# Performance work log

Hardware: AMD Instinct MI355X
Metric: run time of the kernel (lower is better)

## Reference

```python
import jax, jax.numpy as jnp
import numpy as np

EPS_MIN = 1e-8
N_ITER = 50  # solver_iter


def solve_qp_simplex(M, n_iter=N_ITER):
    """Frank-Wolfe min over the simplex of alpha^T M alpha. M: (B,K,K) -> alpha: (B,K)."""
    B, K, _ = M.shape
    alpha0 = jnp.full((B, K), 1.0 / K, dtype=M.dtype)

    def step(alpha, it):
        grad = 2.0 * jnp.einsum('bij,bj->bi', M, alpha)           # (B,K)
        idx = jnp.argmin(grad, axis=1)                             # (B,)
        s = jax.nn.one_hot(idx, K, dtype=alpha.dtype)              # vertex of simplex
        gamma = 2.0 / (it + 2.0)
        return (1.0 - gamma) * alpha + gamma * s, None

    alpha, _ = jax.lax.scan(step, alpha0, jnp.arange(n_iter, dtype=M.dtype))
    return alpha


def _raw_loss(scores, targets, C):
    B, K = scores.shape
    # epsilon = offdiag_mean of C per batch, scaled by 1.0, clamped
    offdiag_mean = (C.sum(axis=(1, 2)) - jnp.trace(C, axis1=1, axis2=2)) / (K * K - K)
    eps = jnp.maximum(offdiag_mean, EPS_MIN)                       # (B,)

    f = 0.5 * scores
    exponent = -(f[:, :, None] + f[:, None, :] + C) / eps[:, None, None]  # (B,K,K)
    shift = exponent.max(axis=(1, 2), keepdims=True)
    logM = exponent - shift
    M = jnp.exp(logM)

    # solver is an implicit layer: non-differentiable by construction
    alpha = jax.lax.stop_gradient(solve_qp_simplex(M, N_ITER))     # (B,K)

    pos = alpha > 0
    loga = jnp.where(pos, jnp.log(jnp.where(pos, alpha, 1.0)), -jnp.inf)
    term = loga[:, :, None] + loga[:, None, :] + logM              # (B,K,K)
    logval = jax.scipy.special.logsumexp(term.reshape(B, K * K), axis=1)
    conjugate = -eps * (logval + shift.reshape(B))

    f_y = jnp.take_along_axis(scores, targets[:, None], axis=1)[:, 0]
    return conjugate - f_y


def setup_inputs() -> dict:
    key = jax.random.key(0)
    k1, k2, k3 = jax.random.split(key, 3)
    B, K = 512, 256
    scores = jax.random.normal(k1, (B, K), dtype=jnp.float32)
    targets = jax.random.randint(k2, (B,), 0, K)
    C = jax.random.uniform(k3, (B, K, K), dtype=jnp.float32)
    return {"scores": scores, "targets": targets, "C": C}


def reference(scores, targets, C):
    return _raw_loss(scores, targets, C).mean()
```

## Files before the change

### kernel.cpp

```cpp
#include <hip/hip_runtime.h>
#include <hip/hip_fp16.h>
#include <math.h>

#define KDIM 256
#define NITER 50
#define REG_H 8192
#define STR 266


__global__ __launch_bounds__(256, 7) void k1_stream(
    const float* __restrict__ scores, const float* __restrict__ C,
    __half* __restrict__ CT,
    float* __restrict__ psum_o, float* __restrict__ ptrace_o, float* __restrict__ pmin_o)
{
    const int blk = blockIdx.x;
    const int b = blk >> 2, chunk = blk & 3;
    const int tid = threadIdx.x, lane = tid & 63, wave = tid >> 6;
    const float4* C4 = (const float4*)(C + (size_t)b * KDIM * KDIM);
    __half* CTb = CT + (size_t)((b*4 + chunk) * 2) * REG_H;

    __shared__ float sf[KDIM];
    __shared__ __half T[32 * STR];
    __shared__ float redS[256], redT[256], redM[256];

    sf[tid] = 0.5f * scores[b*KDIM + tid];
    __syncthreads();

    const int j0 = lane * 4;
    const float fj0 = sf[j0], fj1 = sf[j0+1], fj2 = sf[j0+2], fj3 = sf[j0+3];

    float psum = 0.f, ptrace = 0.f, pmin = INFINITY;

    #pragma unroll
    for (int p = 0; p < 2; ++p) {
        #pragma unroll
        for (int it = 0; it < 8; ++it) {
            const int sl  = it*4 + wave;
            const int row = chunk*64 + p*32 + sl;
            float4 c4 = C4[row*(KDIM/4) + lane];
            const float frow = sf[row];
            psum += (c4.x + c4.y) + (c4.z + c4.w);
            pmin = fminf(pmin, fminf(fminf(frow+fj0+c4.x, frow+fj1+c4.y),
                                     fminf(frow+fj2+c4.z, frow+fj3+c4.w)));
            if ((row >> 2) == lane) {
                int r2 = row & 3;
                ptrace += (r2==0)?c4.x:(r2==1)?c4.y:(r2==2)?c4.z:c4.w;
            }
            __half2 h01, h23;
            h01.x = __float2half_rn(c4.x); h01.y = __float2half_rn(c4.y);
            h23.x = __float2half_rn(c4.z); h23.y = __float2half_rn(c4.w);
            *(__half2*)&T[sl*STR + j0    ] = h01;
            *(__half2*)&T[sl*STR + j0 + 2] = h23;
        }
        __syncthreads();
        {
            __half* dst = CTb + (size_t)p * REG_H;
            const int jr  = tid >> 2;
            const int sl0 = (tid & 3) * 8;
            #pragma unroll
            for (int r = 0; r < 4; ++r) {
                const int j = r*64 + jr;
                uint w[4];
                #pragma unroll
                for (int dw = 0; dw < 4; ++dw) {
                    const uint u0 = (uint)__half_as_ushort(T[(sl0 + dw*2    )*STR + j]);
                    const uint u1 = (uint)__half_as_ushort(T[(sl0 + dw*2 + 1)*STR + j]);
                    w[dw] = u0 | (u1 << 16);
                }
                uint4 v; v.x = w[0]; v.y = w[1]; v.z = w[2]; v.w = w[3];
                *(uint4*)(dst + (size_t)j*32 + sl0) = v;
            }
        }
        __syncthreads();
    }

    redS[tid] = psum; redT[tid] = ptrace; redM[tid] = pmin;
    __syncthreads();
    for (int s = 128; s > 0; s >>= 1) {
        if (tid < s) {
            redS[tid] += redS[tid+s];
            redT[tid] += redT[tid+s];
            redM[tid]  = fminf(redM[tid], redM[tid+s]);
        }
        __syncthreads();
    }
    if (tid == 0) { psum_o[blk] = redS[0]; ptrace_o[blk] = redT[0]; pmin_o[blk] = redM[0]; }
}

__global__ __launch_bounds__(256, 6) void k2_rowsums(
    const float* __restrict__ scores, const __half* __restrict__ CT,
    const float* __restrict__ psum_i, const float* __restrict__ ptrace_i, const float* __restrict__ pmin_i,
    float* __restrict__ prs)
{
    const int blk = blockIdx.x;
    const int b = blk >> 2, jc = blk & 3;
    const int tid = threadIdx.x, lane = tid & 63, wave = tid >> 6;
    const __half* CTb = CT + (size_t)b * 8 * REG_H;

    __shared__ float sf[KDIM];
    __shared__ float part[12];
    __shared__ float bc2[2];
    __shared__ float racc[4][KDIM];

    sf[tid] = 0.5f * scores[b*KDIM + tid];
    if (tid < 12) {
        part[tid] = (tid < 4) ? psum_i[b*4+tid]
                  : (tid < 8) ? ptrace_i[b*4+tid-4]
                              : pmin_i[b*4+tid-8];
    }
    __syncthreads();
    if (tid == 0) {
        float s = part[0]+part[1]+part[2]+part[3];
        float t = part[4]+part[5]+part[6]+part[7];
        float mn = fminf(fminf(part[8],part[9]), fminf(part[10],part[11]));
        bc2[0] = mn;
        bc2[1] = fmaxf((s - t) / (float)(KDIM*KDIM - KDIM), 1e-8f);
    }
    __syncthreads();
    const float minv = bc2[0];
    const float inv_eps = 1.0f / bc2[1];

    const int slot = lane & 15;
    const int jj   = lane >> 4;
    const int p    = slot >> 3;
    const int ilv  = slot & 7;

    float fi[4][4];
    #pragma unroll
    for (int c = 0; c < 4; ++c)
        #pragma unroll
        for (int r = 0; r < 4; ++r)
            fi[c][r] = sf[c*64 + slot*4 + r];

    float acc[4][4] = {{0.f}};
    #pragma unroll
    for (int c = 0; c < 4; ++c) {
        const __half* reg = CTb + (size_t)(c*2 + p) * REG_H;
        #pragma unroll
        for (int jg = 0; jg < 4; ++jg) {
            const int j = jc*64 + jg*16 + wave*4 + jj;
            const float mfj = minv - sf[j];
            const __half2* src = (const __half2*)(reg + (size_t)j*32 + ilv*4);
            __half2 h01 = src[0], h23 = src[1];
            acc[c][0] += __expf((mfj - fi[c][0] - __half2float(h01.x)) * inv_eps);
            acc[c][1] += __expf((mfj - fi[c][1] - __half2float(h01.y)) * inv_eps);
            acc[c][2] += __expf((mfj - fi[c][2] - __half2float(h23.x)) * inv_eps);
            acc[c][3] += __expf((mfj - fi[c][3] - __half2float(h23.y)) * inv_eps);
        }
    }
    #pragma unroll
    for (int c = 0; c < 4; ++c)
        #pragma unroll
        for (int r = 0; r < 4; ++r) {
            acc[c][r] += __shfl_xor(acc[c][r], 16);
            acc[c][r] += __shfl_xor(acc[c][r], 32);
        }
    if (lane < 16) {
        #pragma unroll
        for (int c = 0; c < 4; ++c)
            #pragma unroll
            for (int r = 0; r < 4; ++r)
                racc[wave][c*64 + lane*4 + r] = acc[c][r];
    }
    __syncthreads();
    prs[(size_t)blk*KDIM + tid] = racc[0][tid]+racc[1][tid]+racc[2][tid]+racc[3][tid];
}

__global__ __launch_bounds__(256) void k3_fw(
    const float* __restrict__ scores, const int* __restrict__ targets,
    const __half* __restrict__ CT,
    const float* __restrict__ psum_i, const float* __restrict__ ptrace_i, const float* __restrict__ pmin_i,
    const float* __restrict__ prs, float* __restrict__ lossB)
{
    const int b = blockIdx.x;
    const int tid = threadIdx.x, lane = tid & 63, wave = tid >> 6;
    const __half* CTb = CT + (size_t)b * 8 * REG_H;

    __shared__ float sf[KDIM];
    __shared__ float part[12];
    __shared__ float bc2[2];
    __shared__ float rsL[KDIM];
    __shared__ float aAll[KDIM];
    __shared__ int   wcnt[4];
    __shared__ int   sIdx[64];
    __shared__ float sLog[64];
    __shared__ float wm[4], wsm[4];

    sf[tid] = 0.5f * scores[b*KDIM + tid];
    if (tid < 12) {
        part[tid] = (tid < 4) ? psum_i[b*4+tid]
                  : (tid < 8) ? ptrace_i[b*4+tid-4]
                              : pmin_i[b*4+tid-8];
    }
    rsL[tid] = prs[(size_t)(b*4+0)*KDIM+tid] + prs[(size_t)(b*4+1)*KDIM+tid]
             + prs[(size_t)(b*4+2)*KDIM+tid] + prs[(size_t)(b*4+3)*KDIM+tid];
    __syncthreads();
    if (tid == 0) {
        float s = part[0]+part[1]+part[2]+part[3];
        float t = part[4]+part[5]+part[6]+part[7];
        float mn = fminf(fminf(part[8],part[9]), fminf(part[10],part[11]));
        bc2[0] = mn;
        bc2[1] = fmaxf((s - t) / (float)(KDIM*KDIM - KDIM), 1e-8f);
    }
    __syncthreads();
    const float minv = bc2[0];
    const float eps = bc2[1];
    const float inv_eps = 1.0f / eps;

    if (wave == 0) {
        const float f0 = sf[lane], f1 = sf[lane+64], f2 = sf[lane+128], f3 = sf[lane+192];
        const __half* g0p = CTb + (size_t)(0*2 + (lane>>5))*REG_H + (lane&31);
        const __half* g1p = CTb + (size_t)(1*2 + (lane>>5))*REG_H + (lane&31);
        const __half* g2p = CTb + (size_t)(2*2 + (lane>>5))*REG_H + (lane&31);
        const __half* g3p = CTb + (size_t)(3*2 + (lane>>5))*REG_H + (lane&31);

        float v = rsL[lane]; int vi = lane;
        float t;
        t = rsL[lane+64];  if (t < v) { v = t; vi = lane+64; }
        t = rsL[lane+128]; if (t < v) { v = t; vi = lane+128; }
        t = rsL[lane+192]; if (t < v) { v = t; vi = lane+192; }
        #pragma unroll
        for (int off = 32; off > 0; off >>= 1) {
            float ov = __shfl_xor(v, off);
            int  ovi = __shfl_xor(vi, off);
            if (ov < v || (ov == v && ovi < vi)) { v = ov; vi = ovi; }
        }
        const int idx0 = vi;

        float fidx = sf[idx0];
        float g0 = 2.0f * __expf((minv - (f0 + fidx + __half2float(g0p[(size_t)idx0*32]))) * inv_eps);
        float g1 = 2.0f * __expf((minv - (f1 + fidx + __half2float(g1p[(size_t)idx0*32]))) * inv_eps);
        float g2 = 2.0f * __expf((minv - (f2 + fidx + __half2float(g2p[(size_t)idx0*32]))) * inv_eps);
        float g3 = 2.0f * __expf((minv - (f3 + fidx + __half2float(g3p[(size_t)idx0*32]))) * inv_eps);
        float a0 = (lane     == idx0) ? 1.0f : 0.0f;
        float a1 = (lane+64  == idx0) ? 1.0f : 0.0f;
        float a2 = (lane+128 == idx0) ? 1.0f : 0.0f;
        float a3 = (lane+192 == idx0) ? 1.0f : 0.0f;

        for (int it = 1; it < NITER; ++it) {
            float v2 = g0; int vi2 = lane;
            if (g1 < v2) { v2 = g1; vi2 = lane+64; }
            if (g2 < v2) { v2 = g2; vi2 = lane+128; }
            if (g3 < v2) { v2 = g3; vi2 = lane+192; }
            #pragma unroll
            for (int off = 32; off > 0; off >>= 1) {
                float ov = __shfl_xor(v2, off);
                int  ovi = __shfl_xor(vi2, off);
                if (ov < v2 || (ov == v2 && ovi < vi2)) { v2 = ov; vi2 = ovi; }
            }
            const int idx = vi2;
            const float gamma = 2.0f / ((float)it + 2.0f);
            const float omg = 1.0f - gamma;
            const int which = idx >> 6;
            float fsel = (which==0) ? f0 : (which==1) ? f1 : (which==2) ? f2 : f3;
            const float fidx2 = __shfl(fsel, idx & 63);
            const size_t co = (size_t)idx * 32;
            const float cc0 = __half2float(g0p[co]);
            const float cc1 = __half2float(g1p[co]);
            const float cc2 = __half2float(g2p[co]);
            const float cc3 = __half2float(g3p[co]);
            g0 = omg*g0 + 2.0f*gamma*__expf((minv - (f0 + fidx2 + cc0)) * inv_eps);
            g1 = omg*g1 + 2.0f*gamma*__expf((minv - (f1 + fidx2 + cc1)) * inv_eps);
            g2 = omg*g2 + 2.0f*gamma*__expf((minv - (f2 + fidx2 + cc2)) * inv_eps);
            g3 = omg*g3 + 2.0f*gamma*__expf((minv - (f3 + fidx2 + cc3)) * inv_eps);
            a0 = omg*a0 + ((lane     == idx) ? gamma : 0.0f);
            a1 = omg*a1 + ((lane+64  == idx) ? gamma : 0.0f);
            a2 = omg*a2 + ((lane+128 == idx) ? gamma : 0.0f);
            a3 = omg*a3 + ((lane+192 == idx) ? gamma : 0.0f);
        }
        aAll[lane]     = a0;
        aAll[lane+64]  = a1;
        aAll[lane+128] = a2;
        aAll[lane+192] = a3;
    }
    __syncthreads();

    const float a = aAll[tid];

    unsigned long long mask = __ballot(a > 0.f);
    if (lane == 0) wcnt[wave] = __popcll(mask);
    __syncthreads();
    int off0 = 0;
    for (int w = 0; w < wave; ++w) off0 += wcnt[w];
    const int count = wcnt[0] + wcnt[1] + wcnt[2] + wcnt[3];
    if (a > 0.f) {
        int pos = off0 + __popcll(mask & ((1ull << lane) - 1ull));
        sIdx[pos] = tid;
        sLog[pos] = logf(a);
    }
    __syncthreads();

    float m = -INFINITY, ss = 0.f;
    const int total = count * count;
    for (int p = tid; p < total; p += KDIM) {
        int ii = p / count;
        int jj = p - ii * count;
        int i = sIdx[ii], j = sIdx[jj];
        float cij = __half2float(CTb[(size_t)((i>>6)*2 + ((i>>5)&1))*REG_H + (size_t)j*32 + (i&31)]);
        float lm = (minv - (sf[i] + sf[j] + cij)) * inv_eps;
        float tt = sLog[ii] + sLog[jj] + lm;
        if (tt > m) { ss = ss * __expf(m - tt) + 1.0f; m = tt; }
        else        { ss += __expf(tt - m); }
    }
    #pragma unroll
    for (int off = 32; off > 0; off >>= 1) {
        float om = __shfl_xor(m, off);
        float os = __shfl_xor(ss, off);
        if (os > 0.f) {
            if (ss <= 0.f)   { m = om; ss = os; }
            else if (om > m) { ss = ss*__expf(m-om) + os; m = om; }
            else             { ss += os*__expf(om-m); }
        }
    }
    if (lane == 0) { wm[wave] = m; wsm[wave] = ss; }
    __syncthreads();
    if (tid == 0) {
        float M = wm[0], S = wsm[0];
        #pragma unroll
        for (int w = 1; w < 4; ++w) {
            float om = wm[w], os = wsm[w];
            if (os > 0.f) {
                if (S <= 0.f)    { M = om; S = os; }
                else if (om > M) { S = S*__expf(M-om) + os; M = om; }
                else             { S += os*__expf(om-M); }
            }
        }
        float logval = M + logf(S);
        float shift = -minv * inv_eps;
        float conjugate = -eps * (logval + shift);
        float fy = scores[b*KDIM + targets[b]];
        lossB[b] = conjugate - fy;
    }
}

__global__ __launch_bounds__(512) void cacis_reduce(const float* __restrict__ lossB,
                                                    float* __restrict__ out, int B)
{
    __shared__ float red[512];
    int t = threadIdx.x;
    red[t] = (t < B) ? lossB[t] : 0.f;
    __syncthreads();
    for (int s = 256; s > 0; s >>= 1) { if (t < s) red[t] += red[t+s]; __syncthreads(); }
    if (t == 0) out[0] = red[0] / (float)B;
}

extern "C" void kernel_launch(void* const* d_in, const int* in_sizes, int n_in,
                              void* d_out, int out_size, void* d_ws, size_t ws_size,
                              hipStream_t stream) {
    const float* scores  = (const float*)d_in[0];
    const int*   targets = (const int*)d_in[1];
    const float* C       = (const float*)d_in[2];
    float* out = (float*)d_out;
    const int B = in_sizes[1];

    __half* CT  = (__half*)d_ws;
    float* wsf  = (float*)((char*)d_ws + (size_t)67108864);
    float* psum   = wsf;
    float* ptrace = wsf + 2048;
    float* pmin   = wsf + 4096;
    float* prs    = wsf + 6144;
    float* lossB  = wsf + 6144 + 524288;

    k1_stream <<<B*4, 256, 0, stream>>>(scores, C, CT, psum, ptrace, pmin);
    k2_rowsums<<<B*4, 256, 0, stream>>>(scores, CT, psum, ptrace, pmin, prs);
    k3_fw     <<<B,   256, 0, stream>>>(scores, targets, CT, psum, ptrace, pmin, prs, lossB);
    cacis_reduce<<<1, 512, 0, stream>>>(lossB, out, B);
}
```

Baseline: 114.8 us.

## Compute row sums from fp32 C during transpose pass, split partials into separate kernel

Moves the exp row-sum computation into the pass that writes the fp16 transposed copy, reading C directly in fp32 and reducing rows with wave shuffles. The global statistics (sum, trace, min) get their own lighter first kernel, so the second kernel already knows eps and the min. This removes the separate kernel that re-read the fp16 copy and the 4-way partial row-sum buffer, but C is now streamed twice instead of once.

```diff
diff --git a/kernel.cpp b/kernel.cpp
--- a/kernel.cpp
+++ b/kernel.cpp
@@ -8,28 +8,87 @@
 #define STR 266
 
 
-__global__ __launch_bounds__(256, 7) void k1_stream(
+__global__ __launch_bounds__(256, 8) void k1_partials(
     const float* __restrict__ scores, const float* __restrict__ C,
-    __half* __restrict__ CT,
     float* __restrict__ psum_o, float* __restrict__ ptrace_o, float* __restrict__ pmin_o)
 {
     const int blk = blockIdx.x;
     const int b = blk >> 2, chunk = blk & 3;
     const int tid = threadIdx.x, lane = tid & 63, wave = tid >> 6;
     const float4* C4 = (const float4*)(C + (size_t)b * KDIM * KDIM);
+
+    __shared__ float sf[KDIM];
+    __shared__ float redS[256], redT[256], redM[256];
+    sf[tid] = 0.5f * scores[b*KDIM + tid];
+    __syncthreads();
+
+    const int j0 = lane * 4;
+    const float fj0 = sf[j0], fj1 = sf[j0+1], fj2 = sf[j0+2], fj3 = sf[j0+3];
+
+    const int row0 = chunk * 64;
+    float psum = 0.f, ptrace = 0.f, pmin = INFINITY;
+    #pragma unroll
+    for (int rr = 0; rr < 16; ++rr) {
+        const int row = row0 + wave + rr*4;
+        float4 c4 = C4[row*(KDIM/4) + lane];
+        const float frow = sf[row];
+        psum += (c4.x + c4.y) + (c4.z + c4.w);
+        pmin = fminf(pmin, fminf(fminf(frow+fj0+c4.x, frow+fj1+c4.y),
+                                 fminf(frow+fj2+c4.z, frow+fj3+c4.w)));
+        if ((row >> 2) == lane) {
+            int r2 = row & 3;
+            ptrace += (r2==0)?c4.x:(r2==1)?c4.y:(r2==2)?c4.z:c4.w;
+        }
+    }
+    redS[tid] = psum; redT[tid] = ptrace; redM[tid] = pmin;
+    __syncthreads();
+    for (int s = 128; s > 0; s >>= 1) {
+        if (tid < s) {
+            redS[tid] += redS[tid+s];
+            redT[tid] += redT[tid+s];
+            redM[tid]  = fminf(redM[tid], redM[tid+s]);
+        }
+        __syncthreads();
+    }
+    if (tid == 0) { psum_o[blk] = redS[0]; ptrace_o[blk] = redT[0]; pmin_o[blk] = redM[0]; }
+}
+
+__global__ __launch_bounds__(256, 7) void k2_trowsum(
+    const float* __restrict__ scores, const float* __restrict__ C,
+    const float* __restrict__ psum_i, const float* __restrict__ ptrace_i, const float* __restrict__ pmin_i,
+    __half* __restrict__ CT, float* __restrict__ rs)
+{
+    const int blk = blockIdx.x;
+    const int b = blk >> 2, chunk = blk & 3;
+    const int tid = threadIdx.x, lane = tid & 63, wave = tid >> 6;
+    const float4* C4 = (const float4*)(C + (size_t)b * KDIM * KDIM);
     __half* CTb = CT + (size_t)((b*4 + chunk) * 2) * REG_H;
 
     __shared__ float sf[KDIM];
     __shared__ __half T[32 * STR];
-    __shared__ float redS[256], redT[256], redM[256];
+    __shared__ float part[12];
+    __shared__ float bc2[2];
 
     sf[tid] = 0.5f * scores[b*KDIM + tid];
-    __syncthreads();
+    if (tid < 12) {
+        part[tid] = (tid < 4) ? psum_i[b*4+tid]
+                  : (tid < 8) ? ptrace_i[b*4+tid-4]
+                              : pmin_i[b*4+tid-8];
+    }
+    __syncthreads();
+    if (tid == 0) {
+        float s = part[0]+part[1]+part[2]+part[3];
+        float t = part[4]+part[5]+part[6]+part[7];
+        float mn = fminf(fminf(part[8],part[9]), fminf(part[10],part[11]));
+        bc2[0] = mn;
+        bc2[1] = fmaxf((s - t) / (float)(KDIM*KDIM - KDIM), 1e-8f);
+    }
+    __syncthreads();
+    const float minv = bc2[0];
+    const float inv_eps = 1.0f / bc2[1];
 
     const int j0 = lane * 4;
     const float fj0 = sf[j0], fj1 = sf[j0+1], fj2 = sf[j0+2], fj3 = sf[j0+3];
-
-    float psum = 0.f, ptrace = 0.f, pmin = INFINITY;
 
     #pragma unroll
     for (int p = 0; p < 2; ++p) {
@@ -38,14 +97,14 @@
             const int sl  = it*4 + wave;
             const int row = chunk*64 + p*32 + sl;
             float4 c4 = C4[row*(KDIM/4) + lane];
-            const float frow = sf[row];
-            psum += (c4.x + c4.y) + (c4.z + c4.w);
-            pmin = fminf(pmin, fminf(fminf(frow+fj0+c4.x, frow+fj1+c4.y),
-                                     fminf(frow+fj2+c4.z, frow+fj3+c4.w)));
-            if ((row >> 2) == lane) {
-                int r2 = row & 3;
-                ptrace += (r2==0)?c4.x:(r2==1)?c4.y:(r2==2)?c4.z:c4.w;
-            }
+            const float base = minv - sf[row];
+            float s4 = __expf((base - fj0 - c4.x) * inv_eps)
+                     + __expf((base - fj1 - c4.y) * inv_eps)
+                     + __expf((base - fj2 - c4.z) * inv_eps)
+                     + __expf((base - fj3 - c4.w) * inv_eps);
+            #pragma unroll
+            for (int off = 32; off > 0; off >>= 1) s4 += __shfl_xor(s4, off);
+            if (lane == 0) rs[b*KDIM + row] = s4;
             __half2 h01, h23;
             h01.x = __float2half_rn(c4.x); h01.y = __float2half_rn(c4.y);
             h23.x = __float2half_rn(c4.z); h23.y = __float2half_rn(c4.w);
@@ -73,104 +132,13 @@
         }
         __syncthreads();
     }
-
-    redS[tid] = psum; redT[tid] = ptrace; redM[tid] = pmin;
-    __syncthreads();
-    for (int s = 128; s > 0; s >>= 1) {
-        if (tid < s) {
-            redS[tid] += redS[tid+s];
-            redT[tid] += redT[tid+s];
-            redM[tid]  = fminf(redM[tid], redM[tid+s]);
-        }
-        __syncthreads();
-    }
-    if (tid == 0) { psum_o[blk] = redS[0]; ptrace_o[blk] = redT[0]; pmin_o[blk] = redM[0]; }
-}
-
-__global__ __launch_bounds__(256, 6) void k2_rowsums(
-    const float* __restrict__ scores, const __half* __restrict__ CT,
-    const float* __restrict__ psum_i, const float* __restrict__ ptrace_i, const float* __restrict__ pmin_i,
-    float* __restrict__ prs)
-{
-    const int blk = blockIdx.x;
-    const int b = blk >> 2, jc = blk & 3;
-    const int tid = threadIdx.x, lane = tid & 63, wave = tid >> 6;
-    const __half* CTb = CT + (size_t)b * 8 * REG_H;
-
-    __shared__ float sf[KDIM];
-    __shared__ float part[12];
-    __shared__ float bc2[2];
-    __shared__ float racc[4][KDIM];
-
-    sf[tid] = 0.5f * scores[b*KDIM + tid];
-    if (tid < 12) {
-        part[tid] = (tid < 4) ? psum_i[b*4+tid]
-                  : (tid < 8) ? ptrace_i[b*4+tid-4]
-                              : pmin_i[b*4+tid-8];
-    }
-    __syncthreads();
-    if (tid == 0) {
-        float s = part[0]+part[1]+part[2]+part[3];
-        float t = part[4]+part[5]+part[6]+part[7];
-        float mn = fminf(fminf(part[8],part[9]), fminf(part[10],part[11]));
-        bc2[0] = mn;
-        bc2[1] = fmaxf((s - t) / (float)(KDIM*KDIM - KDIM), 1e-8f);
-    }
-    __syncthreads();
-    const float minv = bc2[0];
-    const float inv_eps = 1.0f / bc2[1];
-
-    const int slot = lane & 15;
-    const int jj   = lane >> 4;
-    const int p    = slot >> 3;
-    const int ilv  = slot & 7;
-
-    float fi[4][4];
-    #pragma unroll
-    for (int c = 0; c < 4; ++c)
-        #pragma unroll
-        for (int r = 0; r < 4; ++r)
-            fi[c][r] = sf[c*64 + slot*4 + r];
-
-    float acc[4][4] = {{0.f}};
-    #pragma unroll
-    for (int c = 0; c < 4; ++c) {
-        const __half* reg = CTb + (size_t)(c*2 + p) * REG_H;
-        #pragma unroll
-        for (int jg = 0; jg < 4; ++jg) {
-            const int j = jc*64 + jg*16 + wave*4 + jj;
-            const float mfj = minv - sf[j];
-            const __half2* src = (const __half2*)(reg + (size_t)j*32 + ilv*4);
-            __half2 h01 = src[0], h23 = src[1];
-            acc[c][0] += __expf((mfj - fi[c][0] - __half2float(h01.x)) * inv_eps);
-            acc[c][1] += __expf((mfj - fi[c][1] - __half2float(h01.y)) * inv_eps);
-            acc[c][2] += __expf((mfj - fi[c][2] - __half2float(h23.x)) * inv_eps);
-            acc[c][3] += __expf((mfj - fi[c][3] - __half2float(h23.y)) * inv_eps);
-        }
-    }
-    #pragma unroll
-    for (int c = 0; c < 4; ++c)
-        #pragma unroll
-        for (int r = 0; r < 4; ++r) {
-            acc[c][r] += __shfl_xor(acc[c][r], 16);
-            acc[c][r] += __shfl_xor(acc[c][r], 32);
-        }
-    if (lane < 16) {
-        #pragma unroll
-        for (int c = 0; c < 4; ++c)
-            #pragma unroll
-            for (int r = 0; r < 4; ++r)
-                racc[wave][c*64 + lane*4 + r] = acc[c][r];
-    }
-    __syncthreads();
-    prs[(size_t)blk*KDIM + tid] = racc[0][tid]+racc[1][tid]+racc[2][tid]+racc[3][tid];
 }
 
 __global__ __launch_bounds__(256) void k3_fw(
     const float* __restrict__ scores, const int* __restrict__ targets,
     const __half* __restrict__ CT,
     const float* __restrict__ psum_i, const float* __restrict__ ptrace_i, const float* __restrict__ pmin_i,
-    const float* __restrict__ prs, float* __restrict__ lossB)
+    const float* __restrict__ rs, float* __restrict__ lossB)
 {
     const int b = blockIdx.x;
     const int tid = threadIdx.x, lane = tid & 63, wave = tid >> 6;
@@ -192,8 +160,7 @@
                   : (tid < 8) ? ptrace_i[b*4+tid-4]
                               : pmin_i[b*4+tid-8];
     }
-    rsL[tid] = prs[(size_t)(b*4+0)*KDIM+tid] + prs[(size_t)(b*4+1)*KDIM+tid]
-             + prs[(size_t)(b*4+2)*KDIM+tid] + prs[(size_t)(b*4+3)*KDIM+tid];
+    rsL[tid] = rs[b*KDIM + tid];
     __syncthreads();
     if (tid == 0) {
         float s = part[0]+part[1]+part[2]+part[3];
@@ -358,11 +325,11 @@
     float* psum   = wsf;
     float* ptrace = wsf + 2048;
     float* pmin   = wsf + 4096;
-    float* prs    = wsf + 6144;
-    float* lossB  = wsf + 6144 + 524288;
-
-    k1_stream <<<B*4, 256, 0, stream>>>(scores, C, CT, psum, ptrace, pmin);
-    k2_rowsums<<<B*4, 256, 0, stream>>>(scores, CT, psum, ptrace, pmin, prs);
-    k3_fw     <<<B,   256, 0, stream>>>(scores, targets, CT, psum, ptrace, pmin, prs, lossB);
+    float* rs     = wsf + 6144;
+    float* lossB  = wsf + 6144 + 131072;
+
+    k1_partials<<<B*4, 256, 0, stream>>>(scores, C, psum, ptrace, pmin);
+    k2_trowsum <<<B*4, 256, 0, stream>>>(scores, C, psum, ptrace, pmin, CT, rs);
+    k3_fw      <<<B,   256, 0, stream>>>(scores, targets, CT, psum, ptrace, pmin, rs, lossB);
     cacis_reduce<<<1, 512, 0, stream>>>(lossB, out, B);
 }
```

New measurement: 124.0 us. 1.08x slower.
